# Performance work log

Hardware: AMD Instinct MI355X
Metric: run time of the kernel (lower is better)

Reference implementation:

```python
import jax, jax.numpy as jnp
import numpy as np

N = 50000
E = 1600000
NEG_SLOPE = 0.2
EPS = 1e-16


def gat_conv(x, src, dst, W, att_src, att_dst, bias):
    # x: [N, F_in]; W: [F_in, H*C]; att_*: [H, C]; bias: [H*C]
    H, C = att_src.shape
    h = (x @ W).reshape(-1, H, C)               # [N, H, C]
    a_src = jnp.sum(h * att_src[None], axis=-1)  # [N, H]
    a_dst = jnp.sum(h * att_dst[None], axis=-1)  # [N, H]
    e = a_src[src] + a_dst[dst]                  # [E, H]
    e = jnp.where(e > 0, e, NEG_SLOPE * e)       # leaky_relu
    # segment softmax over incoming edges of each destination node
    m = jax.ops.segment_max(e, dst, num_segments=N)          # [N, H]
    ex = jnp.exp(e - m[dst])                                  # [E, H]
    s = jax.ops.segment_sum(ex, dst, num_segments=N)          # [N, H]
    alpha = ex / (s[dst] + EPS)                               # [E, H]
    out = jax.ops.segment_sum(h[src] * alpha[:, :, None], dst, num_segments=N)  # [N, H, C]
    return out.reshape(-1, H * C) + bias


def setup_inputs() -> dict:
    key = jax.random.key(0)
    ks = jax.random.split(key, 12)
    x = jax.random.normal(ks[0], (N, 128), dtype=jnp.float32)
    edge_index = jax.random.randint(ks[1], (2, E), 0, N, dtype=jnp.int64)
    W1 = jax.random.normal(ks[2], (128, 128), dtype=jnp.float32) * 0.1
    att_src1 = jax.random.normal(ks[3], (4, 32), dtype=jnp.float32) * 0.1
    att_dst1 = jax.random.normal(ks[4], (4, 32), dtype=jnp.float32) * 0.1
    bias1 = jax.random.normal(ks[5], (128,), dtype=jnp.float32) * 0.1
    W2 = jax.random.normal(ks[6], (128, 64), dtype=jnp.float32) * 0.1
    att_src2 = jax.random.normal(ks[7], (1, 64), dtype=jnp.float32) * 0.1
    att_dst2 = jax.random.normal(ks[8], (1, 64), dtype=jnp.float32) * 0.1
    bias2 = jax.random.normal(ks[9], (64,), dtype=jnp.float32) * 0.1
    return {"x": x, "edge_index": edge_index, "W1": W1, "att_src1": att_src1,
            "att_dst1": att_dst1, "bias1": bias1, "W2": W2, "att_src2": att_src2,
            "att_dst2": att_dst2, "bias2": bias2}


def reference(x, edge_index, W1, att_src1, att_dst1, bias1, W2, att_src2, att_dst2, bias2):
    # GATConv adds self loops by default
    loops = jnp.arange(N, dtype=edge_index.dtype)
    src = jnp.concatenate([edge_index[0], loops])
    dst = jnp.concatenate([edge_index[1], loops])
    # eval mode: dropouts are identity
    h = gat_conv(x, src, dst, W1, att_src1, att_dst1, bias1)
    h = jax.nn.elu(h)
    out = gat_conv(h, src, dst, W2, att_src2, att_dst2, bias2)
    return out
```

## Files before the change

### kernel.cpp

```cpp
#include <hip/hip_runtime.h>
#include <hip/hip_fp16.h>
#include <math.h>


#define NB_BUCKETS 256
#define BCAP 16384

typedef _Float16 half8 __attribute__((ext_vector_type(8)));
typedef float    floatx4 __attribute__((ext_vector_type(4)));

__device__ __forceinline__ unsigned short f2h_bits(float f) {
    return __half_as_ushort(__float2half(f));
}
__device__ __forceinline__ float h2f_lo(unsigned int u) {
    return __half2float(__ushort_as_half((unsigned short)(u & 0xFFFFu)));
}
__device__ __forceinline__ float h2f_hi(unsigned int u) {
    return __half2float(__ushort_as_half((unsigned short)(u >> 16)));
}

__device__ void splitA_body(int bx, const int* __restrict__ eidx,
        unsigned int* __restrict__ tmp, int* __restrict__ coarse_fill,
        int E, int etot, int nb)
{
    __shared__ int hist[NB_BUCKETS];
    __shared__ int gb[NB_BUCKETS];
    __shared__ int cnt2[NB_BUCKETS];
    int t = threadIdx.x;
    if (t < nb) { hist[t] = 0; cnt2[t] = 0; }
    __syncthreads();

    unsigned int val[16];
    int bkt[16];
    int base = bx * 4096;
    #pragma unroll
    for (int i = 0; i < 16; i++) {
        int idx = base + i * 256 + t;
        if (idx < etot) {
            unsigned int s, d;
            if (idx < E) { s = (unsigned int)eidx[idx]; d = (unsigned int)eidx[E + idx]; }
            else         { s = (unsigned int)(idx - E); d = s; }
            val[i] = (d << 16) | s;
            bkt[i] = (int)(d >> 8);
            atomicAdd(&hist[bkt[i]], 1);
        } else {
            bkt[i] = -1;
        }
    }
    __syncthreads();
    if (t < nb) {
        int n = hist[t];
        gb[t] = (n > 0) ? atomicAdd(&coarse_fill[t], n) : 0;
    }
    __syncthreads();
    #pragma unroll
    for (int i = 0; i < 16; i++) {
        if (bkt[i] >= 0) {
            int loc = atomicAdd(&cnt2[bkt[i]], 1);
            tmp[(size_t)bkt[i] * BCAP + gb[bkt[i]] + loc] = val[i];
        }
    }
}

template<int NT, int H, bool AF16>
__device__ void gemm_attn_body(int bx,
        const void* __restrict__ Xv, const float* __restrict__ W,
        const float* __restrict__ att_s, const float* __restrict__ att_d,
        unsigned short* __restrict__ Hf16, float* __restrict__ as_,
        float* __restrict__ ad_, int M)
{
    constexpr int D = NT * 16;
    constexpr int C = D / H;
    __shared__ _Float16 Bs[NT * 4 * 64 * 8];

    int t = threadIdx.x;
    for (int idx = t; idx < 128 * D; idx += 256) {
        int k = idx / D;
        int n = idx - k * D;
        int nt = n >> 4, ks = k >> 5;
        int lane = (((k >> 3) & 3) << 4) | (n & 15);
        int j = k & 7;
        Bs[(((nt * 4 + ks) * 64 + lane) << 3) + j] = (_Float16)W[idx];
    }
    __syncthreads();

    int lane = t & 63;
    int wv = t >> 6;
    int quad = lane >> 4, colL = lane & 15;
    int row0 = bx * 64 + wv * 16;

    int arow = row0 + colL; if (arow > M - 1) arow = M - 1;
    half8 afrag[4];
    if constexpr (AF16) {
        const unsigned short* Xh = (const unsigned short*)Xv;
        #pragma unroll
        for (int ks = 0; ks < 4; ks++)
            afrag[ks] = *(const half8*)(const void*)(Xh + (size_t)arow * 128 + ks * 32 + quad * 8);
    } else {
        const float* Xf = (const float*)Xv;
        #pragma unroll
        for (int ks = 0; ks < 4; ks++) {
            const float* pa = Xf + (size_t)arow * 128 + ks * 32 + quad * 8;
            float4 a0 = *(const float4*)pa;
            float4 a1 = *(const float4*)(pa + 4);
            half8 f;
            f[0] = (_Float16)a0.x; f[1] = (_Float16)a0.y;
            f[2] = (_Float16)a0.z; f[3] = (_Float16)a0.w;
            f[4] = (_Float16)a1.x; f[5] = (_Float16)a1.y;
            f[6] = (_Float16)a1.z; f[7] = (_Float16)a1.w;
            afrag[ks] = f;
        }
    }

    floatx4 acc[NT];
    #pragma unroll
    for (int nt = 0; nt < NT; nt++) {
        floatx4 c = {0.f, 0.f, 0.f, 0.f};
        #pragma unroll
        for (int ks = 0; ks < 4; ks++) {
            half8 b = *(half8*)(void*)&Bs[(((nt * 4 + ks) * 64 + lane) << 3)];
            c = __builtin_amdgcn_mfma_f32_16x16x32_f16(afrag[ks], b, c, 0, 0, 0);
        }
        acc[nt] = c;
    }

    float atts[NT], attd[NT];
    #pragma unroll
    for (int nt = 0; nt < NT; nt++) {
        int ch = nt * 16 + colL;
        atts[nt] = att_s[ch];
        attd[nt] = att_d[ch];
    }
    float ps[H][4], pd[H][4];
    #pragma unroll
    for (int h = 0; h < H; h++)
        #pragma unroll
        for (int r = 0; r < 4; r++) { ps[h][r] = 0.f; pd[h][r] = 0.f; }
    #pragma unroll
    for (int nt = 0; nt < NT; nt++) {
        int h = (nt * 16) / C;
        #pragma unroll
        for (int r = 0; r < 4; r++) {
            ps[h][r] += acc[nt][r] * atts[nt];
            pd[h][r] += acc[nt][r] * attd[nt];
        }
    }
    #pragma unroll
    for (int h = 0; h < H; h++)
        #pragma unroll
        for (int r = 0; r < 4; r++)
            #pragma unroll
            for (int off = 1; off < 16; off <<= 1) {
                ps[h][r] += __shfl_xor(ps[h][r], off);
                pd[h][r] += __shfl_xor(pd[h][r], off);
            }
    if (colL < H) {
        #pragma unroll
        for (int r = 0; r < 4; r++) {
            int row = row0 + quad * 4 + r;
            if (row < M) {
                float vs, vd;
                if constexpr (H == 4) {
                    vs = colL == 0 ? ps[0][r] : colL == 1 ? ps[1][r] : colL == 2 ? ps[2][r] : ps[3][r];
                    vd = colL == 0 ? pd[0][r] : colL == 1 ? pd[1][r] : colL == 2 ? pd[2][r] : pd[3][r];
                } else {
                    vs = ps[0][r]; vd = pd[0][r];
                }
                as_[(size_t)row * H + colL] = vs;
                ad_[(size_t)row * H + colL] = vd;
            }
        }
    }

    #pragma unroll
    for (int r = 0; r < 4; r++) {
        int row = row0 + quad * 4 + r;
        if (row < M) {
            #pragma unroll
            for (int nt = 0; nt < NT; nt++)
                Hf16[(size_t)row * D + nt * 16 + colL] = f2h_bits(acc[nt][r]);
        }
    }
}

__global__ __launch_bounds__(256) void build_and_gemm1_kernel(
        const int* __restrict__ eidx, unsigned int* __restrict__ tmp,
        int* __restrict__ cfill, int E, int etot, int nb,
        const float* __restrict__ x, const float* __restrict__ W1,
        const float* __restrict__ att_s, const float* __restrict__ att_d,
        unsigned short* __restrict__ h1f16, float* __restrict__ as1,
        float* __restrict__ ad1, int M, int nbG)
{
    if ((int)blockIdx.x < nbG)
        gemm_attn_body<8, 4, false>((int)blockIdx.x, x, W1, att_s, att_d,
                                    h1f16, as1, ad1, M);
    else
        splitA_body((int)blockIdx.x - nbG, eidx, tmp, cfill, E, etot, nb);
}

__global__ __launch_bounds__(256) void gemm_attn2_kernel(
        const void* __restrict__ Xv, const float* __restrict__ W,
        const float* __restrict__ att_s, const float* __restrict__ att_d,
        unsigned short* __restrict__ Hf16, float* __restrict__ as_,
        float* __restrict__ ad_, int M)
{
    gemm_attn_body<4, 1, true>((int)blockIdx.x, Xv, W, att_s, att_d, Hf16, as_, ad_, M);
}

__global__ __launch_bounds__(1024) void passB_kernel(const unsigned int* __restrict__ tmp,
        const int* __restrict__ cfill, int* __restrict__ col,
        int* __restrict__ rowp, int N_, int nb, int etot)
{
    __shared__ int sd[256];
    __shared__ int hist2[256];
    __shared__ int scn[256];
    __shared__ int off2[256];
    int b = blockIdx.x;
    int t = threadIdx.x;

    if (t < 256) sd[t] = (t < nb) ? cfill[t] : 0;
    __syncthreads();
    for (int off = 1; off < 256; off <<= 1) {
        int y = 0;
        if (t < 256 && t >= off) y = sd[t - off];
        __syncthreads();
        if (t < 256) sd[t] += y;
        __syncthreads();
    }
    int base = sd[b] - cfill[b];
    int n = cfill[b];
    const unsigned int* seg = tmp + (size_t)b * BCAP;

    if (t < 256) hist2[t] = 0;
    __syncthreads();
    for (int i = t; i < n; i += 1024) {
        unsigned int v = seg[i];
        atomicAdd(&hist2[(v >> 16) & 255], 1);
    }
    __syncthreads();
    int myc = (t < 256) ? hist2[t] : 0;
    if (t < 256) scn[t] = myc;
    __syncthreads();
    for (int off = 1; off < 256; off <<= 1) {
        int y = 0;
        if (t < 256 && t >= off) y = scn[t - off];
        __syncthreads();
        if (t < 256) scn[t] += y;
        __syncthreads();
    }
    if (t < 256) {
        int excl = scn[t] - myc;
        off2[t] = excl;
        int node = b * 256 + t;
        if (node <= N_) rowp[node] = base + excl;
        if (node == N_) rowp[N_] = etot;
    }
    __syncthreads();
    for (int i = t; i < n; i += 1024) {
        unsigned int v = seg[i];
        int bin = (v >> 16) & 255;
        int loc = atomicAdd(&off2[bin], 1);
        col[base + loc] = (int)(v & 0xFFFFu);
    }
}

template<int H, int C, bool ELU_, bool OUTF16>
__global__ __launch_bounds__(256) void aggregate_fused(
        const int* __restrict__ row_ptr, const int* __restrict__ col_src,
        const unsigned short* __restrict__ payload, const float* __restrict__ asv,
        const float* __restrict__ adv, const float* __restrict__ bias,
        void* __restrict__ outv, int nnodes)
{
    constexpr int D = H * C;
    constexpr int CPL = 8;
    constexpr int LPE = D / CPL;
    constexpr int EPI = 64 / LPE;
    __shared__ float2 exs[4][H][65];
    int wave = threadIdx.x >> 6, lane = threadIdx.x & 63;
    int node = blockIdx.x * 4 + wave;
    if (node >= nnodes) return;
    int start = row_ptr[node];
    int deg   = row_ptr[node + 1] - start;
    int li  = lane & (LPE - 1);
    int sub = lane / LPE;
    int myh = (li * CPL) / C;
    int lane_off = li * 16;

    float adh[H];
    #pragma unroll
    for (int h = 0; h < H; h++) adh[h] = adv[(size_t)node * H + h];

    float m[H];
    #pragma unroll
    for (int h = 0; h < H; h++) m[h] = -3.0e38f;
    float acc[CPL];
    #pragma unroll
    for (int k = 0; k < CPL; k++) acc[k] = 0.f;
    float sacc = 0.f;
    const char* pb = (const char*)payload;

    for (int c0 = 0; c0 < deg; c0 += 64) {
        int cnt = deg - c0; if (cnt > 64) cnt = 64;
        int idx = c0 + lane;
        int svec = 0;
        float e[H];
        if (idx < deg) {
            svec = col_src[start + idx];
            if constexpr (H == 4) {
                float4 av = *(const float4*)(asv + (size_t)svec * 4);
                float t0 = av.x + adh[0], t1 = av.y + adh[1];
                float t2 = av.z + adh[2], t3 = av.w + adh[3];
                e[0] = fmaxf(t0, 0.2f * t0); e[1] = fmaxf(t1, 0.2f * t1);
                e[2] = fmaxf(t2, 0.2f * t2); e[3] = fmaxf(t3, 0.2f * t3);
            } else {
                float tt = asv[svec] + adh[0];
                e[0] = fmaxf(tt, 0.2f * tt);
            }
        } else {
            #pragma unroll
            for (int h = 0; h < H; h++) e[h] = -3.0e38f;
        }
        float nm[H];
        #pragma unroll
        for (int h = 0; h < H; h++) {
            float v = e[h];
            #pragma unroll
            for (int off = 32; off >= 1; off >>= 1)
                v = fmaxf(v, __shfl_xor(v, off));
            nm[h] = fmaxf(m[h], v);
        }
        float sc = __expf(m[myh] - nm[myh]);
        sacc *= sc;
        #pragma unroll
        for (int k = 0; k < CPL; k++) acc[k] *= sc;
        #pragma unroll
        for (int h = 0; h < H; h++) m[h] = nm[h];

        unsigned int boff = (unsigned int)svec * (unsigned int)(D * 2);
        float boff_f = __uint_as_float(boff);
        #pragma unroll
        for (int h = 0; h < H; h++) {
            float ex = (idx < deg) ? __expf(e[h] - m[h]) : 0.f;
            exs[wave][h][lane] = make_float2(ex, boff_f);
        }

        int iters = (cnt + EPI - 1) / EPI;
        #pragma unroll 2
        for (int it = 0; it < iters; it++) {
            int el = it * EPI + sub;
            float2 v = exs[wave][myh][el];
            float exj = v.x;
            unsigned int off = __float_as_uint(v.y);
            uint4 hv = *(const uint4*)(const void*)(pb + off + lane_off);
            sacc += exj;
            acc[0] = fmaf(h2f_lo(hv.x), exj, acc[0]);
            acc[1] = fmaf(h2f_hi(hv.x), exj, acc[1]);
            acc[2] = fmaf(h2f_lo(hv.y), exj, acc[2]);
            acc[3] = fmaf(h2f_hi(hv.y), exj, acc[3]);
            acc[4] = fmaf(h2f_lo(hv.z), exj, acc[4]);
            acc[5] = fmaf(h2f_hi(hv.z), exj, acc[5]);
            acc[6] = fmaf(h2f_lo(hv.w), exj, acc[6]);
            acc[7] = fmaf(h2f_hi(hv.w), exj, acc[7]);
        }
    }

    #pragma unroll
    for (int off = LPE; off < 64; off <<= 1) {
        sacc += __shfl_xor(sacc, off);
        #pragma unroll
        for (int k = 0; k < CPL; k++) acc[k] += __shfl_xor(acc[k], off);
    }
    if (sub == 0) {
        float inv = 1.f / (sacc + 1e-16f);
        int ch = li * CPL;
        float r[CPL];
        #pragma unroll
        for (int k = 0; k < CPL; k++) {
            r[k] = acc[k] * inv + bias[ch + k];
            if (ELU_) r[k] = r[k] > 0.f ? r[k] : (__expf(r[k]) - 1.f);
        }
        if constexpr (OUTF16) {
            unsigned short* o = (unsigned short*)outv;
            unsigned int w0 = (unsigned int)f2h_bits(r[0]) | ((unsigned int)f2h_bits(r[1]) << 16);
            unsigned int w1 = (unsigned int)f2h_bits(r[2]) | ((unsigned int)f2h_bits(r[3]) << 16);
            unsigned int w2 = (unsigned int)f2h_bits(r[4]) | ((unsigned int)f2h_bits(r[5]) << 16);
            unsigned int w3 = (unsigned int)f2h_bits(r[6]) | ((unsigned int)f2h_bits(r[7]) << 16);
            uint4 q = { w0, w1, w2, w3 };
            *(uint4*)(void*)(o + (size_t)node * D + ch) = q;
        } else {
            float* o = (float*)outv;
            float4 w0 = { r[0], r[1], r[2], r[3] };
            float4 w1 = { r[4], r[5], r[6], r[7] };
            *(float4*)(o + (size_t)node * D + ch) = w0;
            *(float4*)(o + (size_t)node * D + ch + 4) = w1;
        }
    }
}

extern "C" void kernel_launch(void* const* d_in, const int* in_sizes, int n_in,
                              void* d_out, int out_size, void* d_ws, size_t ws_size,
                              hipStream_t stream)
{
    const float* x        = (const float*)d_in[0];
    const int*   eidx     = (const int*)  d_in[1];
    const float* W1       = (const float*)d_in[2];
    const float* att_src1 = (const float*)d_in[3];
    const float* att_dst1 = (const float*)d_in[4];
    const float* bias1    = (const float*)d_in[5];
    const float* W2       = (const float*)d_in[6];
    const float* att_src2 = (const float*)d_in[7];
    const float* att_dst2 = (const float*)d_in[8];
    const float* bias2    = (const float*)d_in[9];
    float* out = (float*)d_out;

    const int N_ = in_sizes[0] / 128;
    const int E_ = in_sizes[1] / 2;
    const int ET = E_ + N_;
    const int NB = (N_ + 255) / 256;

    char* p = (char*)d_ws;
    auto alloc = [&](size_t bytes) {
        void* r = (void*)p;
        p += ((bytes + 255) / 256) * 256;
        return r;
    };
    int* rowp  = (int*)alloc((size_t)(N_ + 1) * 4);
    int* cfill = (int*)alloc((size_t)NB_BUCKETS * 4);
    int* colidx = (int*)alloc((size_t)ET * 4);
    unsigned int*   tmp   = (unsigned int*)alloc((size_t)NB_BUCKETS * BCAP * 4);
    unsigned short* h1f16 = (unsigned short*)alloc((size_t)N_ * 128 * 2);
    unsigned short* hx16  = (unsigned short*)alloc((size_t)N_ * 128 * 2);
    unsigned short* h2f16 = (unsigned short*)alloc((size_t)N_ * 64 * 2);
    float* as1 = (float*)alloc((size_t)N_ * 4 * 4);
    float* ad1 = (float*)alloc((size_t)N_ * 4 * 4);
    float* as2 = (float*)alloc((size_t)N_ * 4);
    float* ad2 = (float*)alloc((size_t)N_ * 4);
    (void)ws_size; (void)n_in; (void)out_size;

    const int nbG = (N_ + 63) / 64;
    const int nbA = (ET + 4095) / 4096;

    hipMemsetAsync(cfill, 0, (size_t)NB_BUCKETS * 4, stream);
    build_and_gemm1_kernel<<<nbG + nbA, 256, 0, stream>>>(
        eidx, tmp, cfill, E_, ET, NB,
        x, W1, att_src1, att_dst1, h1f16, as1, ad1, N_, nbG);
    passB_kernel<<<NB, 1024, 0, stream>>>(tmp, cfill, colidx, rowp, N_, NB, ET);
    aggregate_fused<4, 32, true, true><<<(N_ + 3) / 4, 256, 0, stream>>>(
        rowp, colidx, h1f16, as1, ad1, bias1, hx16, N_);
    gemm_attn2_kernel<<<nbG, 256, 0, stream>>>(
        hx16, W2, att_src2, att_dst2, h2f16, as2, ad2, N_);
    aggregate_fused<1, 64, false, false><<<(N_ + 3) / 4, 256, 0, stream>>>(
        rowp, colidx, h2f16, as2, ad2, bias2, out, N_);
}
```

Measured before the change: 232.2 us.

## Fuse all stages into one cooperative persistent kernel with grid syncs

Replaces the memset and five separate kernel launches with a single cooperative kernel of 256 blocks of 1024 threads. It runs CSR build, first GEMM, aggregation, second GEMM and final aggregation as grid-stride phases separated by grid.sync. The goal is to remove launch overhead and inter-kernel gaps. In exchange, each CU holds one large block, which may reduce latency hiding for the gather-heavy aggregation, and it relies on no thread returning early before a grid barrier.

```diff
diff --git a/kernel.cpp b/kernel.cpp
--- a/kernel.cpp
+++ b/kernel.cpp
@@ -1,7 +1,10 @@
 #include <hip/hip_runtime.h>
+#include <hip/hip_cooperative_groups.h>
 #include <hip/hip_fp16.h>
 #include <math.h>
 
+namespace cg = cooperative_groups;
+
 
 #define NB_BUCKETS 256
 #define BCAP 16384
@@ -9,6 +12,8 @@
 typedef _Float16 half8 __attribute__((ext_vector_type(8)));
 typedef float    floatx4 __attribute__((ext_vector_type(4)));
 
+struct f2 { float x, y; };
+
 __device__ __forceinline__ unsigned short f2h_bits(float f) {
     return __half_as_ushort(__float2half(f));
 }
@@ -19,23 +24,25 @@
     return __half2float(__ushort_as_half((unsigned short)(u >> 16)));
 }
 
-__device__ void splitA_body(int bx, const int* __restrict__ eidx,
+#define SM_BYTES 33280
+
+__device__ void splitA_body(char* sm, int vb, const int* __restrict__ eidx,
         unsigned int* __restrict__ tmp, int* __restrict__ coarse_fill,
         int E, int etot, int nb)
 {
-    __shared__ int hist[NB_BUCKETS];
-    __shared__ int gb[NB_BUCKETS];
-    __shared__ int cnt2[NB_BUCKETS];
+    int* hist = (int*)sm;
+    int* gb   = hist + 256;
+    int* cnt2 = gb + 256;
     int t = threadIdx.x;
-    if (t < nb) { hist[t] = 0; cnt2[t] = 0; }
-    __syncthreads();
-
-    unsigned int val[16];
-    int bkt[16];
-    int base = bx * 4096;
-    #pragma unroll
-    for (int i = 0; i < 16; i++) {
-        int idx = base + i * 256 + t;
+    if (t < 256) { hist[t] = 0; cnt2[t] = 0; }
+    __syncthreads();
+
+    unsigned int val[4];
+    int bkt[4];
+    int base = vb * 4096;
+    #pragma unroll
+    for (int i = 0; i < 4; i++) {
+        int idx = base + i * 1024 + t;
         if (idx < etot) {
             unsigned int s, d;
             if (idx < E) { s = (unsigned int)eidx[idx]; d = (unsigned int)eidx[E + idx]; }
@@ -54,7 +61,7 @@
     }
     __syncthreads();
     #pragma unroll
-    for (int i = 0; i < 16; i++) {
+    for (int i = 0; i < 4; i++) {
         if (bkt[i] >= 0) {
             int loc = atomicAdd(&cnt2[bkt[i]], 1);
             tmp[(size_t)bkt[i] * BCAP + gb[bkt[i]] + loc] = val[i];
@@ -63,7 +70,7 @@
 }
 
 template<int NT, int H, bool AF16>
-__device__ void gemm_attn_body(int bx,
+__device__ void gemm_body(char* sm, int vb,
         const void* __restrict__ Xv, const float* __restrict__ W,
         const float* __restrict__ att_s, const float* __restrict__ att_d,
         unsigned short* __restrict__ Hf16, float* __restrict__ as_,
@@ -71,10 +78,10 @@
 {
     constexpr int D = NT * 16;
     constexpr int C = D / H;
-    __shared__ _Float16 Bs[NT * 4 * 64 * 8];
+    _Float16* Bs = (_Float16*)sm;
 
     int t = threadIdx.x;
-    for (int idx = t; idx < 128 * D; idx += 256) {
+    for (int idx = t; idx < 128 * D; idx += 1024) {
         int k = idx / D;
         int n = idx - k * D;
         int nt = n >> 4, ks = k >> 5;
@@ -85,9 +92,9 @@
     __syncthreads();
 
     int lane = t & 63;
-    int wv = t >> 6;
+    int wave = t >> 6;
     int quad = lane >> 4, colL = lane & 15;
-    int row0 = bx * 64 + wv * 16;
+    int row0 = vb * 256 + wave * 16;
 
     int arow = row0 + colL; if (arow > M - 1) arow = M - 1;
     half8 afrag[4];
@@ -183,39 +190,14 @@
     }
 }
 
-__global__ __launch_bounds__(256) void build_and_gemm1_kernel(
-        const int* __restrict__ eidx, unsigned int* __restrict__ tmp,
-        int* __restrict__ cfill, int E, int etot, int nb,
-        const float* __restrict__ x, const float* __restrict__ W1,
-        const float* __restrict__ att_s, const float* __restrict__ att_d,
-        unsigned short* __restrict__ h1f16, float* __restrict__ as1,
-        float* __restrict__ ad1, int M, int nbG)
-{
-    if ((int)blockIdx.x < nbG)
-        gemm_attn_body<8, 4, false>((int)blockIdx.x, x, W1, att_s, att_d,
-                                    h1f16, as1, ad1, M);
-    else
-        splitA_body((int)blockIdx.x - nbG, eidx, tmp, cfill, E, etot, nb);
-}
-
-__global__ __launch_bounds__(256) void gemm_attn2_kernel(
-        const void* __restrict__ Xv, const float* __restrict__ W,
-        const float* __restrict__ att_s, const float* __restrict__ att_d,
-        unsigned short* __restrict__ Hf16, float* __restrict__ as_,
-        float* __restrict__ ad_, int M)
-{
-    gemm_attn_body<4, 1, true>((int)blockIdx.x, Xv, W, att_s, att_d, Hf16, as_, ad_, M);
-}
-
-__global__ __launch_bounds__(1024) void passB_kernel(const unsigned int* __restrict__ tmp,
+__device__ void passB_body(char* sm, int b, const unsigned int* __restrict__ tmp,
         const int* __restrict__ cfill, int* __restrict__ col,
         int* __restrict__ rowp, int N_, int nb, int etot)
 {
-    __shared__ int sd[256];
-    __shared__ int hist2[256];
-    __shared__ int scn[256];
-    __shared__ int off2[256];
-    int b = blockIdx.x;
+    int* sd    = (int*)sm;
+    int* hist2 = sd + 256;
+    int* scn   = hist2 + 256;
+    int* off2  = scn + 256;
     int t = threadIdx.x;
 
     if (t < 256) sd[t] = (t < nb) ? cfill[t] : 0;
@@ -265,7 +247,7 @@
 }
 
 template<int H, int C, bool ELU_, bool OUTF16>
-__global__ __launch_bounds__(256) void aggregate_fused(
+__device__ void agg_body(char* sm, int vb,
         const int* __restrict__ row_ptr, const int* __restrict__ col_src,
         const unsigned short* __restrict__ payload, const float* __restrict__ asv,
         const float* __restrict__ adv, const float* __restrict__ bias,
@@ -275,9 +257,9 @@
     constexpr int CPL = 8;
     constexpr int LPE = D / CPL;
     constexpr int EPI = 64 / LPE;
-    __shared__ float2 exs[4][H][65];
+    f2* exs = (f2*)sm;
     int wave = threadIdx.x >> 6, lane = threadIdx.x & 63;
-    int node = blockIdx.x * 4 + wave;
+    int node = vb * 16 + wave;
     if (node >= nnodes) return;
     int start = row_ptr[node];
     int deg   = row_ptr[node + 1] - start;
@@ -285,6 +267,7 @@
     int sub = lane / LPE;
     int myh = (li * CPL) / C;
     int lane_off = li * 16;
+    f2* exw = exs + (size_t)wave * H * 65;
 
     float adh[H];
     #pragma unroll
@@ -341,14 +324,15 @@
         #pragma unroll
         for (int h = 0; h < H; h++) {
             float ex = (idx < deg) ? __expf(e[h] - m[h]) : 0.f;
-            exs[wave][h][lane] = make_float2(ex, boff_f);
+            exw[h * 65 + lane].x = ex;
+            exw[h * 65 + lane].y = boff_f;
         }
 
         int iters = (cnt + EPI - 1) / EPI;
         #pragma unroll 2
         for (int it = 0; it < iters; it++) {
             int el = it * EPI + sub;
-            float2 v = exs[wave][myh][el];
+            f2 v = exw[myh * 65 + el];
             float exj = v.x;
             unsigned int off = __float_as_uint(v.y);
             uint4 hv = *(const uint4*)(const void*)(pb + off + lane_off);
@@ -395,6 +379,67 @@
             *(float4*)(o + (size_t)node * D + ch + 4) = w1;
         }
     }
+}
+
+struct MegaParams {
+    const int* eidx;
+    unsigned int* tmp;
+    int* cfill;
+    int* colidx;
+    int* rowp;
+    const float* x;
+    const float* W1; const float* att_s1; const float* att_d1; const float* bias1;
+    const float* W2; const float* att_s2; const float* att_d2; const float* bias2;
+    unsigned short* h1f16; unsigned short* hx16; unsigned short* h2f16;
+    float* as1; float* ad1; float* as2; float* ad2;
+    float* out;
+    int E, etot, nb, nbA, nbG, N;
+};
+
+__global__ __launch_bounds__(1024, 4) void mega_kernel(MegaParams p)
+{
+    __shared__ __align__(16) char sm[SM_BYTES];
+    cg::grid_group grid = cg::this_grid();
+    const int GB = (int)gridDim.x;
+    int t = threadIdx.x;
+
+    for (int i = (int)blockIdx.x * 1024 + t; i < NB_BUCKETS; i += GB * 1024)
+        p.cfill[i] = 0;
+    grid.sync();
+
+    int tot1 = p.nbA + p.nbG;
+    for (int vb = (int)blockIdx.x; vb < tot1; vb += GB) {
+        __syncthreads();
+        if (vb < p.nbA)
+            splitA_body(sm, vb, p.eidx, p.tmp, p.cfill, p.E, p.etot, p.nb);
+        else
+            gemm_body<8, 4, false>(sm, vb - p.nbA, p.x, p.W1, p.att_s1, p.att_d1,
+                                   p.h1f16, p.as1, p.ad1, p.N);
+    }
+    grid.sync();
+
+    for (int vb = (int)blockIdx.x; vb < p.nb; vb += GB) {
+        __syncthreads();
+        passB_body(sm, vb, p.tmp, p.cfill, p.colidx, p.rowp, p.N, p.nb, p.etot);
+    }
+    grid.sync();
+
+    int nbagg = (p.N + 15) >> 4;
+    for (int vb = (int)blockIdx.x; vb < nbagg; vb += GB)
+        agg_body<4, 32, true, true>(sm, vb, p.rowp, p.colidx, p.h1f16,
+                                    p.as1, p.ad1, p.bias1, p.hx16, p.N);
+    grid.sync();
+
+    for (int vb = (int)blockIdx.x; vb < p.nbG; vb += GB) {
+        __syncthreads();
+        gemm_body<4, 1, true>(sm, vb, p.hx16, p.W2, p.att_s2, p.att_d2,
+                              p.h2f16, p.as2, p.ad2, p.N);
+    }
+    grid.sync();
+
+    for (int vb = (int)blockIdx.x; vb < nbagg; vb += GB)
+        agg_body<1, 64, false, false>(sm, vb, p.rowp, p.colidx, p.h2f16,
+                                      p.as2, p.ad2, p.bias2, p.out, p.N);
 }
 
 extern "C" void kernel_launch(void* const* d_in, const int* in_sizes, int n_in,
@@ -437,18 +482,21 @@
     float* ad2 = (float*)alloc((size_t)N_ * 4);
     (void)ws_size; (void)n_in; (void)out_size;
 
-    const int nbG = (N_ + 63) / 64;
-    const int nbA = (ET + 4095) / 4096;
-
-    hipMemsetAsync(cfill, 0, (size_t)NB_BUCKETS * 4, stream);
-    build_and_gemm1_kernel<<<nbG + nbA, 256, 0, stream>>>(
-        eidx, tmp, cfill, E_, ET, NB,
-        x, W1, att_src1, att_dst1, h1f16, as1, ad1, N_, nbG);
-    passB_kernel<<<NB, 1024, 0, stream>>>(tmp, cfill, colidx, rowp, N_, NB, ET);
-    aggregate_fused<4, 32, true, true><<<(N_ + 3) / 4, 256, 0, stream>>>(
-        rowp, colidx, h1f16, as1, ad1, bias1, hx16, N_);
-    gemm_attn2_kernel<<<nbG, 256, 0, stream>>>(
-        hx16, W2, att_src2, att_dst2, h2f16, as2, ad2, N_);
-    aggregate_fused<1, 64, false, false><<<(N_ + 3) / 4, 256, 0, stream>>>(
-        rowp, colidx, h2f16, as2, ad2, bias2, out, N_);
-}
+    MegaParams mp;
+    mp.eidx = eidx; mp.tmp = tmp; mp.cfill = cfill;
+    mp.colidx = colidx; mp.rowp = rowp;
+    mp.x = x;
+    mp.W1 = W1; mp.att_s1 = att_src1; mp.att_d1 = att_dst1; mp.bias1 = bias1;
+    mp.W2 = W2; mp.att_s2 = att_src2; mp.att_d2 = att_dst2; mp.bias2 = bias2;
+    mp.h1f16 = h1f16; mp.hx16 = hx16; mp.h2f16 = h2f16;
+    mp.as1 = as1; mp.ad1 = ad1; mp.as2 = as2; mp.ad2 = ad2;
+    mp.out = out;
+    mp.E = E_; mp.etot = ET; mp.nb = NB;
+    mp.nbA = (ET + 4095) / 4096;
+    mp.nbG = (N_ + 255) / 256;
+    mp.N = N_;
+
+    void* kargs[] = { &mp };
+    hipLaunchCooperativeKernel((const void*)mega_kernel,
+                               dim3(256), dim3(1024), kargs, 0, stream);
+}
```

Result: slower. 426.5 us (+83.7%).

## Fuse aggregation, second GEMM and aggregation into cooperative persistent kernel

Applied to the files above, without the earlier changes.

Replaces the three tail launches (layer-1 aggregation, layer-2 GEMM, layer-2 aggregation) with one cooperative persistent kernel that loops over virtual blocks and separates the phases with grid-wide syncs. The aim is to remove launch gaps and tail drain between the three kernels. The cost is two grid barriers, a grid capped at 1280 blocks with launch bounds of 4 blocks per CU (which may limit occupancy for the latency-bound gather), and an occupancy query on the host at every call. If the cooperative launch fails, the code falls back to three separate kernels.

```diff
diff --git a/kernel.cpp b/kernel.cpp
--- a/kernel.cpp
+++ b/kernel.cpp
@@ -1,13 +1,18 @@
 #include <hip/hip_runtime.h>
+#include <hip/hip_cooperative_groups.h>
 #include <hip/hip_fp16.h>
 #include <math.h>
 
+namespace cg = cooperative_groups;
+
 
 #define NB_BUCKETS 256
 #define BCAP 16384
 
 typedef _Float16 half8 __attribute__((ext_vector_type(8)));
 typedef float    floatx4 __attribute__((ext_vector_type(4)));
+
+struct f2 { float x, y; };
 
 __device__ __forceinline__ unsigned short f2h_bits(float f) {
     return __half_as_ushort(__float2half(f));
@@ -63,7 +68,7 @@
 }
 
 template<int NT, int H, bool AF16>
-__device__ void gemm_attn_body(int bx,
+__device__ void gemm_attn_body(_Float16* Bs, int bx,
         const void* __restrict__ Xv, const float* __restrict__ W,
         const float* __restrict__ att_s, const float* __restrict__ att_d,
         unsigned short* __restrict__ Hf16, float* __restrict__ as_,
@@ -71,7 +76,6 @@
 {
     constexpr int D = NT * 16;
     constexpr int C = D / H;
-    __shared__ _Float16 Bs[NT * 4 * 64 * 8];
 
     int t = threadIdx.x;
     for (int idx = t; idx < 128 * D; idx += 256) {
@@ -191,20 +195,13 @@
         unsigned short* __restrict__ h1f16, float* __restrict__ as1,
         float* __restrict__ ad1, int M, int nbG)
 {
-    if ((int)blockIdx.x < nbG)
-        gemm_attn_body<8, 4, false>((int)blockIdx.x, x, W1, att_s, att_d,
+    if ((int)blockIdx.x < nbG) {
+        __shared__ _Float16 Bs[8 * 4 * 64 * 8];
+        gemm_attn_body<8, 4, false>(Bs, (int)blockIdx.x, x, W1, att_s, att_d,
                                     h1f16, as1, ad1, M);
-    else
+    } else {
         splitA_body((int)blockIdx.x - nbG, eidx, tmp, cfill, E, etot, nb);
-}
-
-__global__ __launch_bounds__(256) void gemm_attn2_kernel(
-        const void* __restrict__ Xv, const float* __restrict__ W,
-        const float* __restrict__ att_s, const float* __restrict__ att_d,
-        unsigned short* __restrict__ Hf16, float* __restrict__ as_,
-        float* __restrict__ ad_, int M)
-{
-    gemm_attn_body<4, 1, true>((int)blockIdx.x, Xv, W, att_s, att_d, Hf16, as_, ad_, M);
+    }
 }
 
 __global__ __launch_bounds__(1024) void passB_kernel(const unsigned int* __restrict__ tmp,
@@ -265,7 +262,7 @@
 }
 
 template<int H, int C, bool ELU_, bool OUTF16>
-__global__ __launch_bounds__(256) void aggregate_fused(
+__device__ void agg_body(f2* exs, int vb,
         const int* __restrict__ row_ptr, const int* __restrict__ col_src,
         const unsigned short* __restrict__ payload, const float* __restrict__ asv,
         const float* __restrict__ adv, const float* __restrict__ bias,
@@ -275,9 +272,8 @@
     constexpr int CPL = 8;
     constexpr int LPE = D / CPL;
     constexpr int EPI = 64 / LPE;
-    __shared__ float2 exs[4][H][65];
     int wave = threadIdx.x >> 6, lane = threadIdx.x & 63;
-    int node = blockIdx.x * 4 + wave;
+    int node = vb * 4 + wave;
     if (node >= nnodes) return;
     int start = row_ptr[node];
     int deg   = row_ptr[node + 1] - start;
@@ -285,6 +281,7 @@
     int sub = lane / LPE;
     int myh = (li * CPL) / C;
     int lane_off = li * 16;
+    f2* exw = exs + (size_t)wave * H * 65;
 
     float adh[H];
     #pragma unroll
@@ -341,14 +338,15 @@
         #pragma unroll
         for (int h = 0; h < H; h++) {
             float ex = (idx < deg) ? __expf(e[h] - m[h]) : 0.f;
-            exs[wave][h][lane] = make_float2(ex, boff_f);
+            exw[h * 65 + lane].x = ex;
+            exw[h * 65 + lane].y = boff_f;
         }
 
         int iters = (cnt + EPI - 1) / EPI;
         #pragma unroll 2
         for (int it = 0; it < iters; it++) {
             int el = it * EPI + sub;
-            float2 v = exs[wave][myh][el];
+            f2 v = exw[myh * 65 + el];
             float exj = v.x;
             unsigned int off = __float_as_uint(v.y);
             uint4 hv = *(const uint4*)(const void*)(pb + off + lane_off);
@@ -395,6 +393,62 @@
             *(float4*)(o + (size_t)node * D + ch + 4) = w1;
         }
     }
+}
+
+struct TailParams {
+    const int* rowp; const int* colidx;
+    const unsigned short* h1f16;
+    const float* as1; const float* ad1; const float* bias1;
+    unsigned short* hx16;
+    const float* W2; const float* att_s2; const float* att_d2; const float* bias2;
+    unsigned short* h2f16;
+    float* as2; float* ad2;
+    float* out;
+    int N, nbagg, nbG2;
+};
+
+#define TAIL_SM 16640
+
+__global__ __launch_bounds__(256, 4) void tail_mega_kernel(TailParams p)
+{
+    __shared__ __align__(16) char sm[TAIL_SM];
+    cg::grid_group grid = cg::this_grid();
+    const int GB = (int)gridDim.x;
+
+    for (int vb = (int)blockIdx.x; vb < p.nbagg; vb += GB)
+        agg_body<4, 32, true, true>((f2*)sm, vb, p.rowp, p.colidx, p.h1f16,
+                                    p.as1, p.ad1, p.bias1, p.hx16, p.N);
+    grid.sync();
+
+    for (int vb = (int)blockIdx.x; vb < p.nbG2; vb += GB) {
+        __syncthreads();
+        gemm_attn_body<4, 1, true>((_Float16*)sm, vb, p.hx16, p.W2,
+                                   p.att_s2, p.att_d2, p.h2f16, p.as2, p.ad2, p.N);
+    }
+    grid.sync();
+
+    for (int vb = (int)blockIdx.x; vb < p.nbagg; vb += GB)
+        agg_body<1, 64, false, false>((f2*)sm, vb, p.rowp, p.colidx, p.h2f16,
+                                      p.as2, p.ad2, p.bias2, p.out, p.N);
+}
+
+__global__ __launch_bounds__(256) void agg1_kernel(TailParams p)
+{
+    __shared__ __align__(16) char sm[8320];
+    agg_body<4, 32, true, true>((f2*)sm, (int)blockIdx.x, p.rowp, p.colidx,
+                                p.h1f16, p.as1, p.ad1, p.bias1, p.hx16, p.N);
+}
+__global__ __launch_bounds__(256) void gemm2_kernel(TailParams p)
+{
+    __shared__ _Float16 Bs[4 * 4 * 64 * 8];
+    gemm_attn_body<4, 1, true>(Bs, (int)blockIdx.x, p.hx16, p.W2,
+                               p.att_s2, p.att_d2, p.h2f16, p.as2, p.ad2, p.N);
+}
+__global__ __launch_bounds__(256) void agg2_kernel(TailParams p)
+{
+    __shared__ __align__(16) char sm[8320];
+    agg_body<1, 64, false, false>((f2*)sm, (int)blockIdx.x, p.rowp, p.colidx,
+                                  p.h2f16, p.as2, p.ad2, p.bias2, p.out, p.N);
 }
 
 extern "C" void kernel_launch(void* const* d_in, const int* in_sizes, int n_in,
@@ -445,10 +499,33 @@
         eidx, tmp, cfill, E_, ET, NB,
         x, W1, att_src1, att_dst1, h1f16, as1, ad1, N_, nbG);
     passB_kernel<<<NB, 1024, 0, stream>>>(tmp, cfill, colidx, rowp, N_, NB, ET);
-    aggregate_fused<4, 32, true, true><<<(N_ + 3) / 4, 256, 0, stream>>>(
-        rowp, colidx, h1f16, as1, ad1, bias1, hx16, N_);
-    gemm_attn2_kernel<<<nbG, 256, 0, stream>>>(
-        hx16, W2, att_src2, att_dst2, h2f16, as2, ad2, N_);
-    aggregate_fused<1, 64, false, false><<<(N_ + 3) / 4, 256, 0, stream>>>(
-        rowp, colidx, h2f16, as2, ad2, bias2, out, N_);
-}
+
+    TailParams tp;
+    tp.rowp = rowp; tp.colidx = colidx;
+    tp.h1f16 = h1f16; tp.as1 = as1; tp.ad1 = ad1; tp.bias1 = bias1;
+    tp.hx16 = hx16;
+    tp.W2 = W2; tp.att_s2 = att_src2; tp.att_d2 = att_dst2; tp.bias2 = bias2;
+    tp.h2f16 = h2f16; tp.as2 = as2; tp.ad2 = ad2;
+    tp.out = out;
+    tp.N = N_;
+    tp.nbagg = (N_ + 3) / 4;
+    tp.nbG2  = nbG;
+
+    int occ = 0;
+    hipError_t oerr = hipOccupancyMaxActiveBlocksPerMultiprocessor(
+        &occ, (const void*)tail_mega_kernel, 256, 0);
+    bool coop_ok = false;
+    if (oerr == hipSuccess && occ > 0) {
+        int grid = occ * 256;
+        if (grid > 1280) grid = 1280;
+        void* kargs[] = { &tp };
+        hipError_t lerr = hipLaunchCooperativeKernel(
+            (const void*)tail_mega_kernel, dim3(grid), dim3(256), kargs, 0, stream);
+        coop_ok = (lerr == hipSuccess);
+    }
+    if (!coop_ok) {
+        agg1_kernel<<<tp.nbagg, 256, 0, stream>>>(tp);
+        gemm2_kernel<<<tp.nbG2, 256, 0, stream>>>(tp);
+        agg2_kernel<<<tp.nbagg, 256, 0, stream>>>(tp);
+    }
+}
```

New measurement: 468.1 us. +101.6%, slower.
